# Optimization experiments

Measured on AMD Instinct MI355X. Metric: run time of the kernel, lower is better.

## Reference

```python
import jax, jax.numpy as jnp
import numpy as np

EPS = 1e-6
DELTA = 1e-6
GAMMA = 1.0


def setup_inputs() -> dict:
    key = jax.random.key(0)
    ks = jax.random.split(key, 6)
    B, N, D, DDIR, DSIM = 2, 384, 256, 128, 64
    sc = lambda d: 1.0 / np.sqrt(d)
    return {
        "t": jax.random.normal(ks[0], (B, N, D), jnp.float32),
        "Qd": jax.random.normal(ks[1], (D, DDIR), jnp.float32) * sc(D),
        "Kd": jax.random.normal(ks[2], (D, DDIR), jnp.float32) * sc(D),
        "Vd": jax.random.normal(ks[3], (DDIR, D), jnp.float32) * sc(DDIR),
        "Qs": jax.random.normal(ks[4], (D, DSIM), jnp.float32) * sc(D),
        "Ks": jax.random.normal(ks[5], (D, DSIM), jnp.float32) * sc(D),
        "a_l": jnp.ones((1,), jnp.float32),
        "b_l": jnp.zeros((1,), jnp.float32),
    }


def reference(t, Qd, Kd, Vd, Qs, Ks, a_l, b_l):
    B, N, D = t.shape
    d_sim = Qs.shape[1]
    # --- similarity: s_ij = <Qs t_i, Ks t_j>/sqrt(d_sim), then symmetrize ---
    q = t @ Qs  # (B,N,d_sim)
    k = t @ Ks
    s = jnp.einsum('bnd,bmd->bnm', q, k) / jnp.sqrt(jnp.float32(d_sim))
    s = 0.5 * (s + s.transpose(0, 2, 1))
    # --- global z-score over off-diagonal entries (biased var) ---
    eye = jnp.eye(N, dtype=bool)[None]  # (1,N,N)
    cnt = jnp.float32(N * (N - 1))
    mu = jnp.where(eye, 0.0, s).sum((1, 2), keepdims=True) / cnt  # (B,1,1)
    var = jnp.where(eye, 0.0, (s - mu) ** 2).sum((1, 2), keepdims=True) / cnt
    s_hat = (s - mu) / jnp.sqrt(var + EPS)
    tilde_s = a_l.reshape(-1, 1, 1) * s_hat + b_l.reshape(-1, 1, 1)
    # --- gates / mass / inertia / apportioned step ---
    A = jax.nn.sigmoid(tilde_s)                                  # (B,N,N)
    m = 1.0 / (jnp.exp(GAMMA * tilde_s).sum(axis=2) + EPS)       # (B,N)
    w = A * m[:, None, :]                                        # w_ij = m_j A_ij
    alpha = A * (w / (w.sum(axis=2, keepdims=True) + DELTA))     # (B,N,N)
    # --- antisymmetric Hadamard direction gate ---
    qd = t @ Qd  # (B,N,d_dir)
    kd = t @ Kd
    had = qd[:, :, None, :] * kd[:, None, :, :]                  # (B,N,N,d_dir)
    kappa = jnp.einsum('bijr,rd->bijd', had, Vd)                 # (B,N,N,D)
    gate = jax.nn.sigmoid(kappa - kappa.transpose(0, 2, 1, 3))
    Dpair = gate * (t[:, :, None, :] - t[:, None, :, :])         # D_ij = gate*(t_i - t_j)
    # --- exclude self pairs, aggregate update ---
    off = ~eye  # (1,N,N)
    alpha = jnp.where(off, alpha, 0.0)
    Dpair = jnp.where(off[..., None], Dpair, 0.0)
    t_next = t - jnp.einsum('bnm,bnmd->bnd', alpha, Dpair)
    return t_next
```

## Files before the change

### kernel.cpp

```cpp
#include <hip/hip_runtime.h>

#define Bn 2
#define Nn 384
#define Dn 256
#define Rn 128
#define Sn 64
#define BNn (Bn*Nn)
#define NEG_LOG2E -1.44269504088896f

typedef short short8 __attribute__((ext_vector_type(8)));
typedef float f32x4 __attribute__((ext_vector_type(4)));
typedef unsigned int uint;
typedef unsigned short ushort;

static __device__ __forceinline__ float fast_sigmoid(float x) {
    return __builtin_amdgcn_rcpf(1.0f + __expf(-x));
}
static __device__ __forceinline__ ushort f2bf(float f) {
    uint u = __float_as_uint(f);
    uint r = (u + 0x7fffu + ((u >> 16) & 1u)) >> 16;
    return (ushort)r;
}
static __device__ __forceinline__ float bf2f(ushort u) {
    return __uint_as_float(((uint)u) << 16);
}

__global__ __launch_bounds__(256)
void prep_kernel(const float* __restrict__ t,
                 const float* __restrict__ Qd, const float* __restrict__ Kd,
                 const float* __restrict__ Vd,
                 const float* __restrict__ Qs, const float* __restrict__ Ks,
                 float* __restrict__ q, float* __restrict__ k,
                 ushort* __restrict__ qdb, ushort* __restrict__ kdb,
                 ushort* __restrict__ VdT, float* __restrict__ stats) {
    const int bi = blockIdx.x;
    const int tid = threadIdx.x;
    if (bi >= 192) {
        const int idx = (bi - 192) * 256 + tid;
        const int d = idx >> 7, r = idx & 127;
        VdT[idx] = f2bf(NEG_LOG2E * Vd[(size_t)r * Dn + d]);
        if (bi == 319 && tid < 4) stats[tid] = 0.0f;
        return;
    }
    __shared__ float trow[4][Dn];
    const int r0 = bi * 4;
    for (int idx = tid; idx < 4 * Dn; idx += 256)
        trow[idx >> 8][idx & 255] = t[(size_t)r0 * Dn + idx];
    __syncthreads();
    {
        const float* W = (tid < 128) ? Qd : Kd;
        ushort* ob = (tid < 128) ? qdb : kdb;
        const int col = tid & 127;
        float a0 = 0.f, a1 = 0.f, a2 = 0.f, a3 = 0.f;
        for (int kk = 0; kk < Dn; kk += 4) {
            float4 t0 = *(const float4*)&trow[0][kk];
            float4 t1 = *(const float4*)&trow[1][kk];
            float4 t2 = *(const float4*)&trow[2][kk];
            float4 t3 = *(const float4*)&trow[3][kk];
            float w0 = W[(size_t)(kk + 0) * 128 + col];
            float w1 = W[(size_t)(kk + 1) * 128 + col];
            float w2 = W[(size_t)(kk + 2) * 128 + col];
            float w3 = W[(size_t)(kk + 3) * 128 + col];
            a0 += t0.x * w0 + t0.y * w1 + t0.z * w2 + t0.w * w3;
            a1 += t1.x * w0 + t1.y * w1 + t1.z * w2 + t1.w * w3;
            a2 += t2.x * w0 + t2.y * w1 + t2.z * w2 + t2.w * w3;
            a3 += t3.x * w0 + t3.y * w1 + t3.z * w2 + t3.w * w3;
        }
        ob[(size_t)(r0 + 0) * 128 + col] = f2bf(a0);
        ob[(size_t)(r0 + 1) * 128 + col] = f2bf(a1);
        ob[(size_t)(r0 + 2) * 128 + col] = f2bf(a2);
        ob[(size_t)(r0 + 3) * 128 + col] = f2bf(a3);
    }
    if (tid < 128) {
        const float* W = (tid < 64) ? Qs : Ks;
        float* of = (tid < 64) ? q : k;
        const int col = tid & 63;
        float a0 = 0.f, a1 = 0.f, a2 = 0.f, a3 = 0.f;
        for (int kk = 0; kk < Dn; kk += 4) {
            float4 t0 = *(const float4*)&trow[0][kk];
            float4 t1 = *(const float4*)&trow[1][kk];
            float4 t2 = *(const float4*)&trow[2][kk];
            float4 t3 = *(const float4*)&trow[3][kk];
            float w0 = W[(size_t)(kk + 0) * 64 + col];
            float w1 = W[(size_t)(kk + 1) * 64 + col];
            float w2 = W[(size_t)(kk + 2) * 64 + col];
            float w3 = W[(size_t)(kk + 3) * 64 + col];
            a0 += t0.x * w0 + t0.y * w1 + t0.z * w2 + t0.w * w3;
            a1 += t1.x * w0 + t1.y * w1 + t1.z * w2 + t1.w * w3;
            a2 += t2.x * w0 + t2.y * w1 + t2.z * w2 + t2.w * w3;
            a3 += t3.x * w0 + t3.y * w1 + t3.z * w2 + t3.w * w3;
        }
        of[(size_t)(r0 + 0) * 64 + col] = a0;
        of[(size_t)(r0 + 1) * 64 + col] = a1;
        of[(size_t)(r0 + 2) * 64 + col] = a2;
        of[(size_t)(r0 + 3) * 64 + col] = a3;
    }
}

__global__ __launch_bounds__(256)
void ssym_kernel(const float* __restrict__ q, const float* __restrict__ k,
                 float* __restrict__ ssym, float* __restrict__ stats) {
    __shared__ float qi[16][68], ki[16][68], qj[16][68], kj[16][68];
    __shared__ float red[256];
    const int b = blockIdx.z, it = blockIdx.x, jt = blockIdx.y;
    const int tid = threadIdx.x;
    const int r0 = tid >> 6, c = tid & 63;
#pragma unroll
    for (int p = 0; p < 4; ++p) {
        int row = r0 + 4 * p;
        qi[row][c] = q[((size_t)(b * Nn + it * 16 + row)) * Sn + c];
        ki[row][c] = k[((size_t)(b * Nn + it * 16 + row)) * Sn + c];
        qj[row][c] = q[((size_t)(b * Nn + jt * 16 + row)) * Sn + c];
        kj[row][c] = k[((size_t)(b * Nn + jt * 16 + row)) * Sn + c];
    }
    __syncthreads();
    const int ti = tid >> 4, tj = tid & 15;
    float acc = 0.0f;
#pragma unroll
    for (int dd = 0; dd < Sn; dd += 4) {
        float4 a  = *(const float4*)&qi[ti][dd];
        float4 bb = *(const float4*)&kj[tj][dd];
        float4 cc = *(const float4*)&qj[tj][dd];
        float4 d  = *(const float4*)&ki[ti][dd];
        acc += a.x * bb.x + a.y * bb.y + a.z * bb.z + a.w * bb.w
             + cc.x * d.x + cc.y * d.y + cc.z * d.z + cc.w * d.w;
    }
    const float sval = acc * 0.0625f;
    const int gi = it * 16 + ti, gj = jt * 16 + tj;
    ssym[((size_t)(b * Nn + gi)) * Nn + gj] = sval;
    const float v = (gi == gj) ? 0.0f : sval;

    red[tid] = v;
    __syncthreads();
    for (int off = 128; off > 0; off >>= 1) {
        if (tid < off) red[tid] += red[tid + off];
        __syncthreads();
    }
    const float tot_s = red[0];
    __syncthreads();
    red[tid] = v * v;
    __syncthreads();
    for (int off = 128; off > 0; off >>= 1) {
        if (tid < off) red[tid] += red[tid + off];
        __syncthreads();
    }
    if (tid == 0) {
        atomicAdd(&stats[b * 2 + 0], tot_s);
        atomicAdd(&stats[b * 2 + 1], red[0]);
    }
}

__global__ __launch_bounds__(256)
void m_kernel(const float* __restrict__ ssym, const float* __restrict__ stats,
              const float* __restrict__ a_l, const float* __restrict__ b_l,
              float* __restrict__ m) {
    __shared__ float red[256];
    const int row = blockIdx.x;
    const int b = row / Nn;
    const float cnt_inv = 1.0f / (float)(Nn * (Nn - 1));
    const float mu = stats[b * 2 + 0] * cnt_inv;
    const float var = stats[b * 2 + 1] * cnt_inv - mu * mu;
    const float isg = rsqrtf(var + 1e-6f);
    const float a = a_l[0], bbias = b_l[0];
    const int tid = threadIdx.x;
    float sum = __expf(a * (ssym[(size_t)row * Nn + tid] - mu) * isg + bbias);
    if (tid < 128)
        sum += __expf(a * (ssym[(size_t)row * Nn + 256 + tid] - mu) * isg + bbias);
    red[tid] = sum;
    __syncthreads();
    for (int off = 128; off > 0; off >>= 1) {
        if (tid < off) red[tid] += red[tid + off];
        __syncthreads();
    }
    if (tid == 0) m[row] = 1.0f / (red[0] + 1e-6f);
}

__global__ __launch_bounds__(256, 3)
void pair_kernel(const float* __restrict__ t, const float* __restrict__ ssym,
                 const float* __restrict__ mptr, const float* __restrict__ stats,
                 const float* __restrict__ a_l, const float* __restrict__ b_l,
                 const ushort* __restrict__ qdb, const ushort* __restrict__ kdb,
                 const ushort* __restrict__ VdT, float* __restrict__ out) {
    __shared__ ushort h_s[128][136];
    __shared__ float alpha_s[Nn];
    __shared__ float qdi_s[Rn], kdi_s[Rn];
    __shared__ float red[256];

    const int bi = blockIdx.x;
    const int b = bi / Nn;
    const int i = bi - b * Nn;
    const int tid = threadIdx.x;
    const int wave = tid >> 6, lane = tid & 63;
    const int ln = lane & 15, quad = lane >> 4;
    const int wd0 = wave * 64;

    {
        const float cnt_inv = 1.0f / (float)(Nn * (Nn - 1));
        const float mu = stats[b * 2 + 0] * cnt_inv;
        const float var = stats[b * 2 + 1] * cnt_inv - mu * mu;
        const float isg = rsqrtf(var + 1e-6f);
        const float a = a_l[0], bbias = b_l[0];
        float A0, am0, A1 = 0.f, am1 = 0.f;
        {
            float s0 = ssym[(size_t)bi * Nn + tid];
            A0 = fast_sigmoid(a * (s0 - mu) * isg + bbias);
            am0 = A0 * mptr[b * Nn + tid];
        }
        if (tid < 128) {
            float s1 = ssym[(size_t)bi * Nn + 256 + tid];
            A1 = fast_sigmoid(a * (s1 - mu) * isg + bbias);
            am1 = A1 * mptr[b * Nn + 256 + tid];
        }
        red[tid] = am0 + am1;
        __syncthreads();
        for (int off = 128; off > 0; off >>= 1) {
            if (tid < off) red[tid] += red[tid + off];
            __syncthreads();
        }
        const float inv = 1.0f / (red[0] + 1e-6f);
        alpha_s[tid] = (tid == i) ? 0.f : A0 * am0 * inv;
        if (tid < 128)
            alpha_s[256 + tid] = ((256 + tid) == i) ? 0.f : A1 * am1 * inv;
    }
    if (tid < Rn) {
        qdi_s[tid] = bf2f(qdb[(size_t)bi * Rn + tid]);
        kdi_s[tid] = bf2f(kdb[(size_t)bi * Rn + tid]);
    }

    short8 vf[4][4];
#pragma unroll
    for (int dt = 0; dt < 4; ++dt)
#pragma unroll
        for (int ks = 0; ks < 4; ++ks)
            vf[dt][ks] = *(const short8*)&VdT[(size_t)(wd0 + dt * 16 + ln) * Rn + ks * 32 + quad * 8];

    float4 tiv[4];
#pragma unroll
    for (int dt = 0; dt < 4; ++dt)
        tiv[dt] = *(const float4*)&t[(size_t)bi * Dn + wd0 + dt * 16 + quad * 4];

    float4 outac[4];
#pragma unroll
    for (int dt = 0; dt < 4; ++dt) outac[dt] = make_float4(0.f, 0.f, 0.f, 0.f);

    for (int jt0 = 0; jt0 < Nn; jt0 += 128) {
        __syncthreads();
        {
            const int jj = tid >> 1;
            const int r0s = (tid & 1) * 64;
            const size_t rowj = (size_t)(b * Nn + jt0 + jj) * Rn;
            const uint4* qp = (const uint4*)(qdb + rowj + r0s);
            const uint4* kp = (const uint4*)(kdb + rowj + r0s);
#pragma unroll
            for (int c = 0; c < 8; ++c) {
                uint4 qv = qp[c], kv = kp[c];
                uint pk[4];
#pragma unroll
                for (int p = 0; p < 4; ++p) {
                    uint qu = (&qv.x)[p], ku = (&kv.x)[p];
                    float qlo = __uint_as_float(qu << 16);
                    float qhi = __uint_as_float(qu & 0xffff0000u);
                    float klo = __uint_as_float(ku << 16);
                    float khi = __uint_as_float(ku & 0xffff0000u);
                    const int r = r0s + c * 8 + p * 2;
                    float h0 = qdi_s[r]     * klo - kdi_s[r]     * qlo;
                    float h1 = qdi_s[r + 1] * khi - kdi_s[r + 1] * qhi;
                    pk[p] = (uint)f2bf(h0) | ((uint)f2bf(h1) << 16);
                }
                uint4 w; w.x = pk[0]; w.y = pk[1]; w.z = pk[2]; w.w = pk[3];
                *(uint4*)&h_s[jj][r0s + c * 8] = w;
            }
        }
        __syncthreads();

#pragma unroll 1
        for (int jsub = 0; jsub < 8; ++jsub) {
            short8 hf[4];
#pragma unroll
            for (int ks = 0; ks < 4; ++ks)
                hf[ks] = *(const short8*)&h_s[jsub * 16 + ln][ks * 32 + quad * 8];
            const int j = jt0 + jsub * 16 + ln;
            const float al = alpha_s[j];
            const size_t trow_ = (size_t)(b * Nn + j) * Dn;
            float4 tjv[4];
#pragma unroll
            for (int dt = 0; dt < 4; ++dt)
                tjv[dt] = *(const float4*)&t[trow_ + wd0 + dt * 16 + quad * 4];

            f32x4 aA[4], aB[4];
#pragma unroll
            for (int dt = 0; dt < 4; ++dt) {
                f32x4 x = {0.f, 0.f, 0.f, 0.f}, y = {0.f, 0.f, 0.f, 0.f};
                x = __builtin_amdgcn_mfma_f32_16x16x32_bf16(vf[dt][0], hf[0], x, 0, 0, 0);
                y = __builtin_amdgcn_mfma_f32_16x16x32_bf16(vf[dt][1], hf[1], y, 0, 0, 0);
                x = __builtin_amdgcn_mfma_f32_16x16x32_bf16(vf[dt][2], hf[2], x, 0, 0, 0);
                y = __builtin_amdgcn_mfma_f32_16x16x32_bf16(vf[dt][3], hf[3], y, 0, 0, 0);
                aA[dt] = x; aB[dt] = y;
            }
#pragma unroll
            for (int dt = 0; dt < 4; ++dt) {
                const float4 tj = tjv[dt];
                float e0 = aA[dt][0] + aB[dt][0];
                float e1 = aA[dt][1] + aB[dt][1];
                float e2 = aA[dt][2] + aB[dt][2];
                float e3 = aA[dt][3] + aB[dt][3];
                float g0 = __builtin_amdgcn_rcpf(1.0f + __builtin_amdgcn_exp2f(e0));
                float g1 = __builtin_amdgcn_rcpf(1.0f + __builtin_amdgcn_exp2f(e1));
                float g2 = __builtin_amdgcn_rcpf(1.0f + __builtin_amdgcn_exp2f(e2));
                float g3 = __builtin_amdgcn_rcpf(1.0f + __builtin_amdgcn_exp2f(e3));
                outac[dt].x += al * g0 * (tiv[dt].x - tj.x);
                outac[dt].y += al * g1 * (tiv[dt].y - tj.y);
                outac[dt].z += al * g2 * (tiv[dt].z - tj.z);
                outac[dt].w += al * g3 * (tiv[dt].w - tj.w);
            }
        }
    }

#pragma unroll
    for (int dt = 0; dt < 4; ++dt) {
        float4 v = outac[dt];
#pragma unroll
        for (int mask = 1; mask < 16; mask <<= 1) {
            v.x += __shfl_xor(v.x, mask);
            v.y += __shfl_xor(v.y, mask);
            v.z += __shfl_xor(v.z, mask);
            v.w += __shfl_xor(v.w, mask);
        }
        if (ln == 0) {
            float4 o;
            o.x = tiv[dt].x - v.x;
            o.y = tiv[dt].y - v.y;
            o.z = tiv[dt].z - v.z;
            o.w = tiv[dt].w - v.w;
            *(float4*)&out[(size_t)bi * Dn + wd0 + dt * 16 + quad * 4] = o;
        }
    }
}

extern "C" void kernel_launch(void* const* d_in, const int* in_sizes, int n_in,
                              void* d_out, int out_size, void* d_ws, size_t ws_size,
                              hipStream_t stream) {
    const float* t   = (const float*)d_in[0];
    const float* Qd  = (const float*)d_in[1];
    const float* Kd  = (const float*)d_in[2];
    const float* Vd  = (const float*)d_in[3];
    const float* Qs  = (const float*)d_in[4];
    const float* Ks  = (const float*)d_in[5];
    const float* a_l = (const float*)d_in[6];
    const float* b_l = (const float*)d_in[7];
    float* out = (float*)d_out;
    float* ws  = (float*)d_ws;

    float* q     = ws;
    float* k     = q + BNn * Sn;
    float* ssym  = k + BNn * Sn;
    float* m     = ssym + (size_t)BNn * Nn;
    float* stats = m + BNn;
    ushort* qdb  = (ushort*)(stats + 8);
    ushort* kdb  = qdb + (size_t)BNn * Rn;
    ushort* VdT  = kdb + (size_t)BNn * Rn;

    hipLaunchKernelGGL(prep_kernel, dim3(320), dim3(256), 0, stream,
                       t, Qd, Kd, Vd, Qs, Ks, q, k, qdb, kdb, VdT, stats);
    hipLaunchKernelGGL(ssym_kernel, dim3(Nn / 16, Nn / 16, Bn), dim3(256), 0, stream,
                       q, k, ssym, stats);
    hipLaunchKernelGGL(m_kernel, dim3(BNn), dim3(256), 0, stream, ssym, stats, a_l, b_l, m);
    hipLaunchKernelGGL(pair_kernel, dim3(BNn), dim3(256), 0, stream,
                       t, ssym, m, stats, a_l, b_l, qdb, kdb, VdT, out);
}
```

Before: 187.2 us.

## Split pair kernel over j-tiles with atomic accumulation and software prefetch

The pair kernel grid is tripled so each block handles one 128-wide j tile for a row instead of looping over all three. Partial sums are accumulated into the output with atomicAdd, and m_kernel now initializes out with t. Within each tile, the h_s fragments, t_j rows and alpha for the next 16-row subtile are prefetched into registers while the current subtile computes, and launch bounds rise to 4 blocks per SM. In exchange, every block now redoes the alpha row computation and the VdT fragment loads, adds atomic traffic, and gives up bitwise determinism.

Result: slower. 324.8 us (+73.5%).

```diff
diff --git a/kernel.cpp b/kernel.cpp
--- a/kernel.cpp
+++ b/kernel.cpp
@@ -153,6 +153,7 @@
 __global__ __launch_bounds__(256)
 void m_kernel(const float* __restrict__ ssym, const float* __restrict__ stats,
               const float* __restrict__ a_l, const float* __restrict__ b_l,
+              const float* __restrict__ t, float* __restrict__ out,
               float* __restrict__ m) {
     __shared__ float red[256];
     const int row = blockIdx.x;
@@ -163,6 +164,7 @@
     const float isg = rsqrtf(var + 1e-6f);
     const float a = a_l[0], bbias = b_l[0];
     const int tid = threadIdx.x;
+    out[(size_t)row * Dn + tid] = t[(size_t)row * Dn + tid];
     float sum = __expf(a * (ssym[(size_t)row * Nn + tid] - mu) * isg + bbias);
     if (tid < 128)
         sum += __expf(a * (ssym[(size_t)row * Nn + 256 + tid] - mu) * isg + bbias);
@@ -175,7 +177,7 @@
     if (tid == 0) m[row] = 1.0f / (red[0] + 1e-6f);
 }
 
-__global__ __launch_bounds__(256, 3)
+__global__ __launch_bounds__(256, 4)
 void pair_kernel(const float* __restrict__ t, const float* __restrict__ ssym,
                  const float* __restrict__ mptr, const float* __restrict__ stats,
                  const float* __restrict__ a_l, const float* __restrict__ b_l,
@@ -186,13 +188,30 @@
     __shared__ float qdi_s[Rn], kdi_s[Rn];
     __shared__ float red[256];
 
-    const int bi = blockIdx.x;
+    const int bx = blockIdx.x;
+    const int tile = bx >> 10 < 0 ? 0 : bx / BNn;
+    const int bi = bx - tile * BNn;
+    const int jt0 = tile * 128;
     const int b = bi / Nn;
     const int i = bi - b * Nn;
     const int tid = threadIdx.x;
     const int wave = tid >> 6, lane = tid & 63;
     const int ln = lane & 15, quad = lane >> 4;
     const int wd0 = wave * 64;
+
+    const int jj = tid >> 1;
+    const int r0s = (tid & 1) * 64;
+    const size_t rowj = (size_t)(b * Nn + jt0 + jj) * Rn;
+    const uint4* qp = (const uint4*)(qdb + rowj + r0s);
+    const uint4* kp = (const uint4*)(kdb + rowj + r0s);
+    uint4 qv[8], kv[8];
+#pragma unroll
+    for (int c = 0; c < 8; ++c) { qv[c] = qp[c]; kv[c] = kp[c]; }
+
+    if (tid < Rn) {
+        qdi_s[tid] = bf2f(qdb[(size_t)bi * Rn + tid]);
+        kdi_s[tid] = bf2f(kdb[(size_t)bi * Rn + tid]);
+    }
 
     {
         const float cnt_inv = 1.0f / (float)(Nn * (Nn - 1));
@@ -222,9 +241,24 @@
         if (tid < 128)
             alpha_s[256 + tid] = ((256 + tid) == i) ? 0.f : A1 * am1 * inv;
     }
-    if (tid < Rn) {
-        qdi_s[tid] = bf2f(qdb[(size_t)bi * Rn + tid]);
-        kdi_s[tid] = bf2f(kdb[(size_t)bi * Rn + tid]);
+
+#pragma unroll
+    for (int c = 0; c < 8; ++c) {
+        uint pk[4];
+#pragma unroll
+        for (int p = 0; p < 4; ++p) {
+            uint qu = (&qv[c].x)[p], ku = (&kv[c].x)[p];
+            float qlo = __uint_as_float(qu << 16);
+            float qhi = __uint_as_float(qu & 0xffff0000u);
+            float klo = __uint_as_float(ku << 16);
+            float khi = __uint_as_float(ku & 0xffff0000u);
+            const int r = r0s + c * 8 + p * 2;
+            float h0 = qdi_s[r]     * klo - kdi_s[r]     * qlo;
+            float h1 = qdi_s[r + 1] * khi - kdi_s[r + 1] * qhi;
+            pk[p] = (uint)f2bf(h0) | ((uint)f2bf(h1) << 16);
+        }
+        uint4 w; w.x = pk[0]; w.y = pk[1]; w.z = pk[2]; w.w = pk[3];
+        *(uint4*)&h_s[jj][r0s + c * 8] = w;
     }
 
     short8 vf[4][4];
@@ -243,77 +277,71 @@
 #pragma unroll
     for (int dt = 0; dt < 4; ++dt) outac[dt] = make_float4(0.f, 0.f, 0.f, 0.f);
 
-    for (int jt0 = 0; jt0 < Nn; jt0 += 128) {
-        __syncthreads();
-        {
-            const int jj = tid >> 1;
-            const int r0s = (tid & 1) * 64;
-            const size_t rowj = (size_t)(b * Nn + jt0 + jj) * Rn;
-            const uint4* qp = (const uint4*)(qdb + rowj + r0s);
-            const uint4* kp = (const uint4*)(kdb + rowj + r0s);
-#pragma unroll
-            for (int c = 0; c < 8; ++c) {
-                uint4 qv = qp[c], kv = kp[c];
-                uint pk[4];
-#pragma unroll
-                for (int p = 0; p < 4; ++p) {
-                    uint qu = (&qv.x)[p], ku = (&kv.x)[p];
-                    float qlo = __uint_as_float(qu << 16);
-                    float qhi = __uint_as_float(qu & 0xffff0000u);
-                    float klo = __uint_as_float(ku << 16);
-                    float khi = __uint_as_float(ku & 0xffff0000u);
-                    const int r = r0s + c * 8 + p * 2;
-                    float h0 = qdi_s[r]     * klo - kdi_s[r]     * qlo;
-                    float h1 = qdi_s[r + 1] * khi - kdi_s[r + 1] * qhi;
-                    pk[p] = (uint)f2bf(h0) | ((uint)f2bf(h1) << 16);
-                }
-                uint4 w; w.x = pk[0]; w.y = pk[1]; w.z = pk[2]; w.w = pk[3];
-                *(uint4*)&h_s[jj][r0s + c * 8] = w;
-            }
-        }
-        __syncthreads();
+    __syncthreads();
+
+    short8 hf_c[4];
+    float4 tjv_c[4];
+    float al_c;
+    {
+        const int j = jt0 + ln;
+#pragma unroll
+        for (int ks = 0; ks < 4; ++ks)
+            hf_c[ks] = *(const short8*)&h_s[ln][ks * 32 + quad * 8];
+        al_c = alpha_s[j];
+        const size_t trow_ = (size_t)(b * Nn + j) * Dn;
+#pragma unroll
+        for (int dt = 0; dt < 4; ++dt)
+            tjv_c[dt] = *(const float4*)&t[trow_ + wd0 + dt * 16 + quad * 4];
+    }
 
 #pragma unroll 1
-        for (int jsub = 0; jsub < 8; ++jsub) {
-            short8 hf[4];
+    for (int jsub = 0; jsub < 8; ++jsub) {
+        short8 hf_n[4];
+        float4 tjv_n[4];
+        float al_n = 0.f;
+        if (jsub < 7) {
+            const int jn = jt0 + (jsub + 1) * 16 + ln;
 #pragma unroll
             for (int ks = 0; ks < 4; ++ks)
-                hf[ks] = *(const short8*)&h_s[jsub * 16 + ln][ks * 32 + quad * 8];
-            const int j = jt0 + jsub * 16 + ln;
-            const float al = alpha_s[j];
-            const size_t trow_ = (size_t)(b * Nn + j) * Dn;
-            float4 tjv[4];
+                hf_n[ks] = *(const short8*)&h_s[(jsub + 1) * 16 + ln][ks * 32 + quad * 8];
+            al_n = alpha_s[jn];
+            const size_t trow_ = (size_t)(b * Nn + jn) * Dn;
 #pragma unroll
             for (int dt = 0; dt < 4; ++dt)
-                tjv[dt] = *(const float4*)&t[trow_ + wd0 + dt * 16 + quad * 4];
-
-            f32x4 aA[4], aB[4];
-#pragma unroll
-            for (int dt = 0; dt < 4; ++dt) {
-                f32x4 x = {0.f, 0.f, 0.f, 0.f}, y = {0.f, 0.f, 0.f, 0.f};
-                x = __builtin_amdgcn_mfma_f32_16x16x32_bf16(vf[dt][0], hf[0], x, 0, 0, 0);
-                y = __builtin_amdgcn_mfma_f32_16x16x32_bf16(vf[dt][1], hf[1], y, 0, 0, 0);
-                x = __builtin_amdgcn_mfma_f32_16x16x32_bf16(vf[dt][2], hf[2], x, 0, 0, 0);
-                y = __builtin_amdgcn_mfma_f32_16x16x32_bf16(vf[dt][3], hf[3], y, 0, 0, 0);
-                aA[dt] = x; aB[dt] = y;
-            }
-#pragma unroll
-            for (int dt = 0; dt < 4; ++dt) {
-                const float4 tj = tjv[dt];
-                float e0 = aA[dt][0] + aB[dt][0];
-                float e1 = aA[dt][1] + aB[dt][1];
-                float e2 = aA[dt][2] + aB[dt][2];
-                float e3 = aA[dt][3] + aB[dt][3];
-                float g0 = __builtin_amdgcn_rcpf(1.0f + __builtin_amdgcn_exp2f(e0));
-                float g1 = __builtin_amdgcn_rcpf(1.0f + __builtin_amdgcn_exp2f(e1));
-                float g2 = __builtin_amdgcn_rcpf(1.0f + __builtin_amdgcn_exp2f(e2));
-                float g3 = __builtin_amdgcn_rcpf(1.0f + __builtin_amdgcn_exp2f(e3));
-                outac[dt].x += al * g0 * (tiv[dt].x - tj.x);
-                outac[dt].y += al * g1 * (tiv[dt].y - tj.y);
-                outac[dt].z += al * g2 * (tiv[dt].z - tj.z);
-                outac[dt].w += al * g3 * (tiv[dt].w - tj.w);
-            }
-        }
+                tjv_n[dt] = *(const float4*)&t[trow_ + wd0 + dt * 16 + quad * 4];
+        }
+
+        f32x4 aA[4], aB[4];
+#pragma unroll
+        for (int dt = 0; dt < 4; ++dt) {
+            f32x4 x = {0.f, 0.f, 0.f, 0.f}, y = {0.f, 0.f, 0.f, 0.f};
+            x = __builtin_amdgcn_mfma_f32_16x16x32_bf16(vf[dt][0], hf_c[0], x, 0, 0, 0);
+            y = __builtin_amdgcn_mfma_f32_16x16x32_bf16(vf[dt][1], hf_c[1], y, 0, 0, 0);
+            x = __builtin_amdgcn_mfma_f32_16x16x32_bf16(vf[dt][2], hf_c[2], x, 0, 0, 0);
+            y = __builtin_amdgcn_mfma_f32_16x16x32_bf16(vf[dt][3], hf_c[3], y, 0, 0, 0);
+            aA[dt] = x; aB[dt] = y;
+        }
+#pragma unroll
+        for (int dt = 0; dt < 4; ++dt) {
+            const float4 tj = tjv_c[dt];
+            float e0 = aA[dt][0] + aB[dt][0];
+            float e1 = aA[dt][1] + aB[dt][1];
+            float e2 = aA[dt][2] + aB[dt][2];
+            float e3 = aA[dt][3] + aB[dt][3];
+            float g0 = __builtin_amdgcn_rcpf(1.0f + __builtin_amdgcn_exp2f(e0));
+            float g1 = __builtin_amdgcn_rcpf(1.0f + __builtin_amdgcn_exp2f(e1));
+            float g2 = __builtin_amdgcn_rcpf(1.0f + __builtin_amdgcn_exp2f(e2));
+            float g3 = __builtin_amdgcn_rcpf(1.0f + __builtin_amdgcn_exp2f(e3));
+            outac[dt].x += al_c * g0 * (tiv[dt].x - tj.x);
+            outac[dt].y += al_c * g1 * (tiv[dt].y - tj.y);
+            outac[dt].z += al_c * g2 * (tiv[dt].z - tj.z);
+            outac[dt].w += al_c * g3 * (tiv[dt].w - tj.w);
+        }
+#pragma unroll
+        for (int ks = 0; ks < 4; ++ks) hf_c[ks] = hf_n[ks];
+#pragma unroll
+        for (int dt = 0; dt < 4; ++dt) tjv_c[dt] = tjv_n[dt];
+        al_c = al_n;
     }
 
 #pragma unroll
@@ -327,12 +355,11 @@
             v.w += __shfl_xor(v.w, mask);
         }
         if (ln == 0) {
-            float4 o;
-            o.x = tiv[dt].x - v.x;
-            o.y = tiv[dt].y - v.y;
-            o.z = tiv[dt].z - v.z;
-            o.w = tiv[dt].w - v.w;
-            *(float4*)&out[(size_t)bi * Dn + wd0 + dt * 16 + quad * 4] = o;
+            float* op = &out[(size_t)bi * Dn + wd0 + dt * 16 + quad * 4];
+            atomicAdd(op + 0, -v.x);
+            atomicAdd(op + 1, -v.y);
+            atomicAdd(op + 2, -v.z);
+            atomicAdd(op + 3, -v.w);
         }
     }
 }
@@ -364,7 +391,8 @@
                        t, Qd, Kd, Vd, Qs, Ks, q, k, qdb, kdb, VdT, stats);
     hipLaunchKernelGGL(ssym_kernel, dim3(Nn / 16, Nn / 16, Bn), dim3(256), 0, stream,
                        q, k, ssym, stats);
-    hipLaunchKernelGGL(m_kernel, dim3(BNn), dim3(256), 0, stream, ssym, stats, a_l, b_l, m);
-    hipLaunchKernelGGL(pair_kernel, dim3(BNn), dim3(256), 0, stream,
+    hipLaunchKernelGGL(m_kernel, dim3(BNn), dim3(256), 0, stream,
+                       ssym, stats, a_l, b_l, t, out, m);
+    hipLaunchKernelGGL(pair_kernel, dim3(3 * BNn), dim3(256), 0, stream,
                        t, ssym, m, stats, a_l, b_l, qdb, kdb, VdT, out);
 }
```
